# Kernel optimization log

Hardware: AMD Instinct MI355X
Metric: run time of the kernel (lower is better)

## Reference

```python
import jax, jax.numpy as jnp
import numpy as np
import math

EMBED_DIM = 1024
NUM_HEADS = 16
HEAD_DIM = EMBED_DIM // NUM_HEADS          # 64
SUB_HEAD_DIM = HEAD_DIM // 2               # 32
SCALING = 1.0 / math.sqrt(SUB_HEAD_DIM)
LAMBDA_INIT = 0.8 - 0.6 * math.exp(-0.3 * 0)  # layer_idx = 0 -> 0.2


def setup_inputs() -> dict:
    key = jax.random.key(0)
    ks = jax.random.split(key, 10)
    B, T, D = 2, 2048, EMBED_DIM
    xav = math.sqrt(6.0 / (D + D))  # xavier_uniform bound for square-ish mats
    return {
        "query": jax.random.normal(ks[0], (B, T, D), jnp.float32),
        "key": jax.random.normal(ks[1], (B, T, D), jnp.float32),
        "value": jax.random.normal(ks[2], (B, T, D), jnp.float32),
        "in_proj_weight": jax.random.uniform(ks[3], (3 * D, D), jnp.float32, -xav, xav),
        "in_proj_bias": jnp.zeros((3 * D,), jnp.float32),
        "out_proj_weight": jax.random.uniform(ks[4], (D, D), jnp.float32, -xav, xav),
        "out_proj_bias": jnp.zeros((D,), jnp.float32),
        "lambda_q1": 0.1 * jax.random.normal(ks[5], (SUB_HEAD_DIM,), jnp.float32),
        "lambda_k1": 0.1 * jax.random.normal(ks[6], (SUB_HEAD_DIM,), jnp.float32),
        "lambda_q2": 0.1 * jax.random.normal(ks[7], (SUB_HEAD_DIM,), jnp.float32),
        "lambda_k2": 0.1 * jax.random.normal(ks[8], (SUB_HEAD_DIM,), jnp.float32),
    }


def reference(query, key, value, in_proj_weight, in_proj_bias,
              out_proj_weight, out_proj_bias,
              lambda_q1, lambda_k1, lambda_q2, lambda_k2):
    B, T, D = query.shape
    S = key.shape[1]
    H, hd, sd = NUM_HEADS, HEAD_DIM, SUB_HEAD_DIM

    qw, kw, vw = jnp.split(in_proj_weight, 3, axis=0)
    qb, kb, vb = jnp.split(in_proj_bias, 3, axis=0)
    q = query @ qw.T + qb
    k = key @ kw.T + kb
    v = value @ vw.T + vb

    # [B, H, T, head_dim]
    q = q.reshape(B, T, H, hd).transpose(0, 2, 1, 3)
    k = k.reshape(B, S, H, hd).transpose(0, 2, 1, 3)
    v = v.reshape(B, S, H, hd).transpose(0, 2, 1, 3)

    q1, q2 = q[..., :sd], q[..., sd:]
    k1, k2 = k[..., :sd], k[..., sd:]

    logits_1 = jnp.einsum('bhtd,bhsd->bhts', q1, k1) * SCALING
    logits_2 = jnp.einsum('bhtd,bhsd->bhts', q2, k2) * SCALING

    a1 = jax.nn.softmax(logits_1, axis=-1)
    a2 = jax.nn.softmax(logits_2, axis=-1)

    lam = (jnp.exp(jnp.dot(lambda_q1, lambda_k1))
           - jnp.exp(jnp.dot(lambda_q2, lambda_k2)) + LAMBDA_INIT)

    diff_weights = a1 - lam * a2
    attn_output = jnp.einsum('bhts,bhsd->bhtd', diff_weights, v)
    attn_output = attn_output * (1.0 - LAMBDA_INIT)

    attn_output = attn_output.transpose(0, 2, 1, 3).reshape(B, T, D)
    output = attn_output @ out_proj_weight.T + out_proj_bias
    return output
```

## Files before the change

kernel.cpp:

```cpp
#include <hip/hip_runtime.h>
#include <cstdint>
#include <cstddef>

typedef unsigned short u16;
typedef __attribute__((ext_vector_type(8))) short bf16x8;
typedef __attribute__((ext_vector_type(4))) short bf16x4;
typedef __attribute__((ext_vector_type(4))) float f32x4;

__device__ __forceinline__ u16 f2bf(float f) {
  uint32_t u = __float_as_uint(f);
  u += 0x7fffu + ((u >> 16) & 1u);
  return (u16)(u >> 16);
}

__device__ __forceinline__ short f2bfs(float f) {
  __bf16 h = (__bf16)f;
  return __builtin_bit_cast(short, h);
}

__device__ __forceinline__ float bf2f(u16 u) {
  return __uint_as_float(((uint32_t)u) << 16);
}

#define MFMA16(a, b, c) __builtin_amdgcn_mfma_f32_16x16x32_bf16((a), (b), (c), 0, 0, 0)

__device__ __forceinline__ float ex2(float x) {
#if __has_builtin(__builtin_amdgcn_exp2f)
  return __builtin_amdgcn_exp2f(x);
#else
  return exp2f(x);
#endif
}

__global__ __launch_bounds__(256) void cvt3_kernel(const float* __restrict__ q,
                                                   const float* __restrict__ k,
                                                   const float* __restrict__ v,
                                                   u16* __restrict__ out, int n8) {
  int i = blockIdx.x * blockDim.x + threadIdx.x;
  if (i >= n8) return;
  const float* src = blockIdx.y == 0 ? q : (blockIdx.y == 1 ? k : v);
  u16* dst = out + (size_t)blockIdx.y * n8 * 8;
  const float4* p = (const float4*)src;
  float4 a = p[i * 2], b = p[i * 2 + 1];
  u16 o[8] = {f2bf(a.x), f2bf(a.y), f2bf(a.z), f2bf(a.w),
              f2bf(b.x), f2bf(b.y), f2bf(b.z), f2bf(b.w)};
  *(int4*)(dst + (size_t)i * 8) = *(const int4*)o;
}

__global__ __launch_bounds__(256) void cvtw_kernel(const float* __restrict__ w0,
                                                   const float* __restrict__ w1,
                                                   u16* __restrict__ o0,
                                                   u16* __restrict__ o1,
                                                   int n8_0, int n8_1) {
  int i = blockIdx.x * blockDim.x + threadIdx.x;
  const float* src;
  u16* dst;
  if (blockIdx.y == 0) {
    if (i >= n8_0) return;
    src = w0; dst = o0;
  } else {
    if (i >= n8_1) return;
    src = w1; dst = o1;
  }
  const float4* p = (const float4*)src;
  float4 a = p[i * 2], b = p[i * 2 + 1];
  u16 o[8] = {f2bf(a.x), f2bf(a.y), f2bf(a.z), f2bf(a.w),
              f2bf(b.x), f2bf(b.y), f2bf(b.z), f2bf(b.w)};
  *(int4*)(dst + (size_t)i * 8) = *(const int4*)o;
}

template <typename OUT_T, bool SPLIT_A>
__global__ __launch_bounds__(256) void gemm_bt(const u16* __restrict__ Abase,
                                               const u16* __restrict__ B,
                                               const float* __restrict__ bias,
                                               OUT_T* __restrict__ C,
                                               u16* __restrict__ QH, u16* __restrict__ KH,
                                               u16* __restrict__ VT,
                                               int M, int N, int K) {
  __shared__ u16 As[128][68];
  __shared__ u16 Bs[128][68];
  const int nb = blockIdx.x, mb = blockIdx.y;
  const int t = threadIdx.x;
  const u16* A = Abase + (SPLIT_A ? (size_t)(nb >> 3) * (size_t)M * K : (size_t)0);
  const int w = t >> 6, lane = t & 63;
  const int wr = w >> 1, wc = w & 1;
  const int lr = lane & 15, lk = lane >> 4;
  const f32x4 zero4 = {0.f, 0.f, 0.f, 0.f};
  f32x4 acc[4][4];
#pragma unroll
  for (int i = 0; i < 4; ++i)
#pragma unroll
    for (int j = 0; j < 4; ++j) acc[i][j] = zero4;

  const int srow = t >> 3;
  const int scol = (t & 7) << 3;
  const u16* Ap = A + (size_t)(mb * 128 + srow) * K + scol;
  const u16* Bp = B + (size_t)(nb * 128 + srow) * K + scol;

  for (int k0 = 0; k0 < K; k0 += 64) {
    __syncthreads();
#pragma unroll
    for (int j = 0; j < 4; ++j) {
      *(int4*)&As[srow + 32 * j][scol] = *(const int4*)(Ap + (size_t)(32 * j) * K + k0);
      *(int4*)&Bs[srow + 32 * j][scol] = *(const int4*)(Bp + (size_t)(32 * j) * K + k0);
    }
    __syncthreads();
#pragma unroll
    for (int kk = 0; kk < 2; ++kk) {
      bf16x8 af[4], bfr[4];
#pragma unroll
      for (int mf = 0; mf < 4; ++mf)
        af[mf] = *(const bf16x8*)&As[wr * 64 + mf * 16 + lr][kk * 32 + lk * 8];
#pragma unroll
      for (int nf = 0; nf < 4; ++nf)
        bfr[nf] = *(const bf16x8*)&Bs[wc * 64 + nf * 16 + lr][kk * 32 + lk * 8];
#pragma unroll
      for (int mf = 0; mf < 4; ++mf)
#pragma unroll
        for (int nf = 0; nf < 4; ++nf) acc[mf][nf] = MFMA16(af[mf], bfr[nf], acc[mf][nf]);
    }
  }

  if constexpr (SPLIT_A) {
    const int third = nb >> 3;
    const int bb = mb >> 4;
#pragma unroll
    for (int nf = 0; nf < 4; ++nf) {
      const int col = nb * 128 + wc * 64 + nf * 16 + lr;
      const int c = col & 1023;
      const int h = c >> 6, d = c & 63;
      const float bv = bias[col];
      u16* qk = (third == 0 ? QH : KH) + (size_t)(bb * 16 + h) * 2048 * 64;
      u16* vt = VT + ((size_t)(bb * 16 + h) * 64 + d) * 2048;
#pragma unroll
      for (int mf = 0; mf < 4; ++mf) {
        const int row0 = mb * 128 + wr * 64 + mf * 16 + lk * 4;
        const int s0 = row0 & 2047;
        if (third < 2) {
#pragma unroll
          for (int r = 0; r < 4; ++r)
            qk[(size_t)(s0 + r) * 64 + d] = f2bf(acc[mf][nf][r] + bv);
        } else {
          u16 tmp[4];
#pragma unroll
          for (int r = 0; r < 4; ++r) tmp[r] = f2bf(acc[mf][nf][r] + bv);
          *(uint2*)&vt[s0] = *(const uint2*)tmp;
        }
      }
    }
  } else {
#pragma unroll
    for (int nf = 0; nf < 4; ++nf) {
      const int col = nb * 128 + wc * 64 + nf * 16 + lr;
      const float bv = bias[col];
#pragma unroll
      for (int mf = 0; mf < 4; ++mf) {
        const int row0 = mb * 128 + wr * 64 + mf * 16 + lk * 4;
#pragma unroll
        for (int r = 0; r < 4; ++r)
          ((float*)C)[(size_t)(row0 + r) * N + col] = acc[mf][nf][r] + bv;
      }
    }
  }
}

__global__ __launch_bounds__(512, 2) void diff_attn(const u16* __restrict__ QH,
                                                    const u16* __restrict__ KH,
                                                    const u16* __restrict__ VT,
                                                    const float* __restrict__ lq1,
                                                    const float* __restrict__ lk1,
                                                    const float* __restrict__ lq2,
                                                    const float* __restrict__ lk2,
                                                    u16* __restrict__ ATTN) {
  __shared__ u16 Ks[64][68];
  __shared__ u16 Vs[64][68];
  const int t = threadIdx.x;
  const int id = blockIdx.x;
  const int swz = (id & 7) * 64 + (id >> 3);
  const int qt = swz & 15, bh = swz >> 4;
  const int b = bh >> 4, h = bh & 15;
  const int w = t >> 6, lane = t & 63;
  const int lr = lane & 15, lk = lane >> 4;
  const float QSC = 0.17677669529663687f * 1.4426950408889634f;

  float dd1 = 0.f, dd2 = 0.f;
  for (int i = 0; i < 32; ++i) { dd1 += lq1[i] * lk1[i]; dd2 += lq2[i] * lk2[i]; }
  const float lam = __expf(dd1) - __expf(dd2) + 0.2f;

  const int srow = t >> 3;
  const int scol = (t & 7) << 3;
  const int krow = (srow & 32) | ((srow & 4) << 2) | ((srow & 24) >> 1) | (srow & 3);
  const u16* qh = QH + (size_t)(b * 16 + h) * 2048 * 64;
  const u16* kh = KH + (size_t)(b * 16 + h) * 2048 * 64;
  const u16* vt = VT + (size_t)(b * 16 + h) * 64 * 2048;

  bf16x8 qa[2];
#pragma unroll
  for (int hh = 0; hh < 2; ++hh) {
    bf16x8 q = *(const bf16x8*)(qh + (size_t)(qt * 128 + w * 16 + lr) * 64 + hh * 32 + lk * 8);
#pragma unroll
    for (int i = 0; i < 8; ++i) q[i] = f2bfs(bf2f((u16)q[i]) * QSC);
    qa[hh] = q;
  }

  const f32x4 zero4 = {0.f, 0.f, 0.f, 0.f};
  f32x4 O[2][4], Ol[2];
#pragma unroll
  for (int hh = 0; hh < 2; ++hh) {
    Ol[hh] = zero4;
#pragma unroll
    for (int df = 0; df < 4; ++df) O[hh][df] = zero4;
  }
  bf16x8 vone8;
#pragma unroll
  for (int i = 0; i < 8; ++i) vone8[i] = (short)0x3F80;

  const u16* kp = kh + (size_t)srow * 64 + scol;
  const u16* vp = vt + (size_t)srow * 2048 + scol;

  int4 kA = *(const int4*)kp;
  int4 vA = *(const int4*)vp;
  int4 kB, vB;

  for (int it = 0; it < 32; ++it) {
    __syncthreads();
    *(int4*)&Ks[krow][scol] = kA;
    *(int4*)&Vs[srow][scol] = vA;
    if (it < 31) {
      const int s1 = (it + 1) * 64;
      kB = *(const int4*)(kp + (size_t)s1 * 64);
      vB = *(const int4*)(vp + s1);
    }
    __syncthreads();

    bf16x8 pk8[2][2];
#pragma unroll
    for (int hh = 0; hh < 2; ++hh) {
      f32x4 St[4];
#pragma unroll
      for (int nf = 0; nf < 4; ++nf) {
        bf16x8 kb = *(const bf16x8*)&Ks[nf * 16 + lr][hh * 32 + lk * 8];
        St[nf] = MFMA16(kb, qa[hh], zero4);
      }
#pragma unroll
      for (int j = 0; j < 2; ++j) {
        bf16x8 p;
#pragma unroll
        for (int a = 0; a < 2; ++a)
#pragma unroll
          for (int r = 0; r < 4; ++r)
            p[a * 4 + r] = f2bfs(ex2(St[2 * j + a][r]));
        pk8[hh][j] = p;
      }
    }

    __builtin_amdgcn_s_setprio(1);
#pragma unroll
    for (int j = 0; j < 2; ++j) {
      const bf16x8 pa0 = pk8[0][j], pa1 = pk8[1][j];
#pragma unroll
      for (int df = 0; df < 4; ++df) {
        bf16x8 vb = *(const bf16x8*)&Vs[df * 16 + lr][j * 32 + lk * 8];
        O[0][df] = MFMA16(pa0, vb, O[0][df]);
        O[1][df] = MFMA16(pa1, vb, O[1][df]);
      }
      Ol[0] = MFMA16(pa0, vone8, Ol[0]);
      Ol[1] = MFMA16(pa1, vone8, Ol[1]);
    }
    __builtin_amdgcn_s_setprio(0);

    kA = kB; vA = vB;
  }

  float i1[4], i2[4];
#pragma unroll
  for (int r = 0; r < 4; ++r) {
    i1[r] = 1.f / Ol[0][r];
    i2[r] = 1.f / Ol[1][r];
  }
  const size_t qrow0 = (size_t)b * 2048 + (size_t)qt * 128;
#pragma unroll
  for (int df = 0; df < 4; ++df) {
    const int col = h * 64 + df * 16 + lr;
#pragma unroll
    for (int r = 0; r < 4; ++r) {
      const size_t row = qrow0 + w * 16 + lk * 4 + r;
      float v = 0.8f * (O[0][df][r] * i1[r] - lam * O[1][df][r] * i2[r]);
      ATTN[row * 1024 + col] = f2bf(v);
    }
  }
}

extern "C" void kernel_launch(void* const* d_in, const int* in_sizes, int n_in,
                              void* d_out, int out_size, void* d_ws, size_t ws_size,
                              hipStream_t stream) {
  (void)in_sizes; (void)n_in; (void)out_size; (void)ws_size;
  const float* query = (const float*)d_in[0];
  const float* key_  = (const float*)d_in[1];
  const float* value = (const float*)d_in[2];
  const float* ipw   = (const float*)d_in[3];
  const float* ipb   = (const float*)d_in[4];
  const float* opw   = (const float*)d_in[5];
  const float* opb   = (const float*)d_in[6];
  const float* lq1   = (const float*)d_in[7];
  const float* lk1   = (const float*)d_in[8];
  const float* lq2   = (const float*)d_in[9];
  const float* lk2   = (const float*)d_in[10];

  const int M = 4096, D = 1024;
  u16* X    = (u16*)d_ws;
  u16* Wqkv = X + (size_t)3 * M * D;
  u16* Wout = Wqkv + (size_t)3 * D * D;
  u16* QH   = Wout + (size_t)D * D;
  u16* KH   = QH + (size_t)M * D;
  u16* VT   = KH + (size_t)M * D;
  u16* ATTN = VT + (size_t)M * D;

  {
    int n8 = (int)((size_t)M * D / 8);
    cvt3_kernel<<<dim3((n8 + 255) / 256, 3), dim3(256), 0, stream>>>(
        query, key_, value, X, n8);
  }
  {
    int n8_0 = (int)((size_t)3 * D * D / 8);
    int n8_1 = (int)((size_t)D * D / 8);
    cvtw_kernel<<<dim3((n8_0 + 255) / 256, 2), dim3(256), 0, stream>>>(
        ipw, opw, Wqkv, Wout, n8_0, n8_1);
  }

  gemm_bt<u16, true><<<dim3(24, 32), dim3(256), 0, stream>>>(
      X, Wqkv, ipb, (u16*)nullptr, QH, KH, VT, M, 3 * D, D);
  diff_attn<<<dim3(512), dim3(512), 0, stream>>>(QH, KH, VT, lq1, lk1, lq2, lk2, ATTN);
  gemm_bt<float, false><<<dim3(8, 32), dim3(256), 0, stream>>>(
      ATTN, Wout, opb, (float*)d_out, nullptr, nullptr, nullptr, M, D, D);
}
```

Before: 140.0 us.

## Merge conversion kernels, retile output GEMM to 128x64, prioritize QK MFMAs

The two fp32-to-bf16 conversion kernels become one five-way launch, removing a kernel launch. The output projection gets its own GEMM kernel with a 128x64 tile, doubling the block count from 256 to 512 so more of the GPU's compute units are busy. The attention loop also raises wave priority around the QK MFMA issue. In exchange, the smaller output tile has lower arithmetic intensity and reloads more A data per block.

```diff
diff --git a/kernel.cpp b/kernel.cpp
--- a/kernel.cpp
+++ b/kernel.cpp
@@ -32,14 +32,30 @@
 #endif
 }
 
-__global__ __launch_bounds__(256) void cvt3_kernel(const float* __restrict__ q,
+__global__ __launch_bounds__(256) void cvt5_kernel(const float* __restrict__ q,
                                                    const float* __restrict__ k,
                                                    const float* __restrict__ v,
-                                                   u16* __restrict__ out, int n8) {
+                                                   const float* __restrict__ w0,
+                                                   const float* __restrict__ w1,
+                                                   u16* __restrict__ X,
+                                                   u16* __restrict__ Wqkv,
+                                                   u16* __restrict__ Wout,
+                                                   int n8i, int n8w, int n8o) {
   int i = blockIdx.x * blockDim.x + threadIdx.x;
-  if (i >= n8) return;
-  const float* src = blockIdx.y == 0 ? q : (blockIdx.y == 1 ? k : v);
-  u16* dst = out + (size_t)blockIdx.y * n8 * 8;
+  const int y = blockIdx.y;
+  const float* src;
+  u16* dst;
+  if (y < 3) {
+    if (i >= n8i) return;
+    src = (y == 0) ? q : (y == 1 ? k : v);
+    dst = X + (size_t)y * n8i * 8;
+  } else if (y == 3) {
+    if (i >= n8w) return;
+    src = w0; dst = Wqkv;
+  } else {
+    if (i >= n8o) return;
+    src = w1; dst = Wout;
+  }
   const float4* p = (const float4*)src;
   float4 a = p[i * 2], b = p[i * 2 + 1];
   u16 o[8] = {f2bf(a.x), f2bf(a.y), f2bf(a.z), f2bf(a.w),
@@ -47,41 +63,17 @@
   *(int4*)(dst + (size_t)i * 8) = *(const int4*)o;
 }
 
-__global__ __launch_bounds__(256) void cvtw_kernel(const float* __restrict__ w0,
-                                                   const float* __restrict__ w1,
-                                                   u16* __restrict__ o0,
-                                                   u16* __restrict__ o1,
-                                                   int n8_0, int n8_1) {
-  int i = blockIdx.x * blockDim.x + threadIdx.x;
-  const float* src;
-  u16* dst;
-  if (blockIdx.y == 0) {
-    if (i >= n8_0) return;
-    src = w0; dst = o0;
-  } else {
-    if (i >= n8_1) return;
-    src = w1; dst = o1;
-  }
-  const float4* p = (const float4*)src;
-  float4 a = p[i * 2], b = p[i * 2 + 1];
-  u16 o[8] = {f2bf(a.x), f2bf(a.y), f2bf(a.z), f2bf(a.w),
-              f2bf(b.x), f2bf(b.y), f2bf(b.z), f2bf(b.w)};
-  *(int4*)(dst + (size_t)i * 8) = *(const int4*)o;
-}
-
-template <typename OUT_T, bool SPLIT_A>
-__global__ __launch_bounds__(256) void gemm_bt(const u16* __restrict__ Abase,
-                                               const u16* __restrict__ B,
-                                               const float* __restrict__ bias,
-                                               OUT_T* __restrict__ C,
-                                               u16* __restrict__ QH, u16* __restrict__ KH,
-                                               u16* __restrict__ VT,
-                                               int M, int N, int K) {
+__global__ __launch_bounds__(256) void gemm_qkv(const u16* __restrict__ Abase,
+                                                const u16* __restrict__ B,
+                                                const float* __restrict__ bias,
+                                                u16* __restrict__ QH, u16* __restrict__ KH,
+                                                u16* __restrict__ VT,
+                                                int M, int N, int K) {
   __shared__ u16 As[128][68];
   __shared__ u16 Bs[128][68];
   const int nb = blockIdx.x, mb = blockIdx.y;
   const int t = threadIdx.x;
-  const u16* A = Abase + (SPLIT_A ? (size_t)(nb >> 3) * (size_t)M * K : (size_t)0);
+  const u16* A = Abase + (size_t)(nb >> 3) * (size_t)M * K;
   const int w = t >> 6, lane = t & 63;
   const int wr = w >> 1, wc = w & 1;
   const int lr = lane & 15, lk = lane >> 4;
@@ -121,45 +113,92 @@
     }
   }
 
-  if constexpr (SPLIT_A) {
-    const int third = nb >> 3;
-    const int bb = mb >> 4;
-#pragma unroll
-    for (int nf = 0; nf < 4; ++nf) {
-      const int col = nb * 128 + wc * 64 + nf * 16 + lr;
-      const int c = col & 1023;
-      const int h = c >> 6, d = c & 63;
-      const float bv = bias[col];
-      u16* qk = (third == 0 ? QH : KH) + (size_t)(bb * 16 + h) * 2048 * 64;
-      u16* vt = VT + ((size_t)(bb * 16 + h) * 64 + d) * 2048;
-#pragma unroll
-      for (int mf = 0; mf < 4; ++mf) {
-        const int row0 = mb * 128 + wr * 64 + mf * 16 + lk * 4;
-        const int s0 = row0 & 2047;
-        if (third < 2) {
-#pragma unroll
-          for (int r = 0; r < 4; ++r)
-            qk[(size_t)(s0 + r) * 64 + d] = f2bf(acc[mf][nf][r] + bv);
-        } else {
-          u16 tmp[4];
-#pragma unroll
-          for (int r = 0; r < 4; ++r) tmp[r] = f2bf(acc[mf][nf][r] + bv);
-          *(uint2*)&vt[s0] = *(const uint2*)tmp;
-        }
+  const int third = nb >> 3;
+  const int bb = mb >> 4;
+#pragma unroll
+  for (int nf = 0; nf < 4; ++nf) {
+    const int col = nb * 128 + wc * 64 + nf * 16 + lr;
+    const int c = col & 1023;
+    const int h = c >> 6, d = c & 63;
+    const float bv = bias[col];
+    u16* qk = (third == 0 ? QH : KH) + (size_t)(bb * 16 + h) * 2048 * 64;
+    u16* vt = VT + ((size_t)(bb * 16 + h) * 64 + d) * 2048;
+#pragma unroll
+    for (int mf = 0; mf < 4; ++mf) {
+      const int row0 = mb * 128 + wr * 64 + mf * 16 + lk * 4;
+      const int s0 = row0 & 2047;
+      if (third < 2) {
+#pragma unroll
+        for (int r = 0; r < 4; ++r)
+          qk[(size_t)(s0 + r) * 64 + d] = f2bf(acc[mf][nf][r] + bv);
+      } else {
+        u16 tmp[4];
+#pragma unroll
+        for (int r = 0; r < 4; ++r) tmp[r] = f2bf(acc[mf][nf][r] + bv);
+        *(uint2*)&vt[s0] = *(const uint2*)tmp;
       }
     }
-  } else {
-#pragma unroll
-    for (int nf = 0; nf < 4; ++nf) {
-      const int col = nb * 128 + wc * 64 + nf * 16 + lr;
-      const float bv = bias[col];
-#pragma unroll
-      for (int mf = 0; mf < 4; ++mf) {
-        const int row0 = mb * 128 + wr * 64 + mf * 16 + lk * 4;
-#pragma unroll
-        for (int r = 0; r < 4; ++r)
-          ((float*)C)[(size_t)(row0 + r) * N + col] = acc[mf][nf][r] + bv;
-      }
+  }
+}
+
+__global__ __launch_bounds__(256) void gemm_out(const u16* __restrict__ A,
+                                                const u16* __restrict__ B,
+                                                const float* __restrict__ bias,
+                                                float* __restrict__ C,
+                                                int M, int N, int K) {
+  __shared__ u16 As[128][68];
+  __shared__ u16 Bs[64][68];
+  const int nb = blockIdx.x, mb = blockIdx.y;
+  const int t = threadIdx.x;
+  const int w = t >> 6, lane = t & 63;
+  const int lr = lane & 15, lk = lane >> 4;
+  const f32x4 zero4 = {0.f, 0.f, 0.f, 0.f};
+  f32x4 acc[2][4];
+#pragma unroll
+  for (int i = 0; i < 2; ++i)
+#pragma unroll
+    for (int j = 0; j < 4; ++j) acc[i][j] = zero4;
+
+  const int srow = t >> 3;
+  const int scol = (t & 7) << 3;
+  const u16* Ap = A + (size_t)(mb * 128 + srow) * K + scol;
+  const u16* Bp = B + (size_t)(nb * 64 + srow) * K + scol;
+
+  for (int k0 = 0; k0 < K; k0 += 64) {
+    __syncthreads();
+#pragma unroll
+    for (int j = 0; j < 4; ++j)
+      *(int4*)&As[srow + 32 * j][scol] = *(const int4*)(Ap + (size_t)(32 * j) * K + k0);
+#pragma unroll
+    for (int j = 0; j < 2; ++j)
+      *(int4*)&Bs[srow + 32 * j][scol] = *(const int4*)(Bp + (size_t)(32 * j) * K + k0);
+    __syncthreads();
+#pragma unroll
+    for (int kk = 0; kk < 2; ++kk) {
+      bf16x8 af[2], bfr[4];
+#pragma unroll
+      for (int mf = 0; mf < 2; ++mf)
+        af[mf] = *(const bf16x8*)&As[w * 32 + mf * 16 + lr][kk * 32 + lk * 8];
+#pragma unroll
+      for (int nf = 0; nf < 4; ++nf)
+        bfr[nf] = *(const bf16x8*)&Bs[nf * 16 + lr][kk * 32 + lk * 8];
+#pragma unroll
+      for (int mf = 0; mf < 2; ++mf)
+#pragma unroll
+        for (int nf = 0; nf < 4; ++nf) acc[mf][nf] = MFMA16(af[mf], bfr[nf], acc[mf][nf]);
+    }
+  }
+
+#pragma unroll
+  for (int nf = 0; nf < 4; ++nf) {
+    const int col = nb * 64 + nf * 16 + lr;
+    const float bv = bias[col];
+#pragma unroll
+    for (int mf = 0; mf < 2; ++mf) {
+      const int row0 = mb * 128 + w * 32 + mf * 16 + lk * 4;
+#pragma unroll
+      for (int r = 0; r < 4; ++r)
+        C[(size_t)(row0 + r) * N + col] = acc[mf][nf][r] + bv;
     }
   }
 }
@@ -237,11 +276,13 @@
 #pragma unroll
     for (int hh = 0; hh < 2; ++hh) {
       f32x4 St[4];
+      __builtin_amdgcn_s_setprio(1);
 #pragma unroll
       for (int nf = 0; nf < 4; ++nf) {
         bf16x8 kb = *(const bf16x8*)&Ks[nf * 16 + lr][hh * 32 + lk * 8];
         St[nf] = MFMA16(kb, qa[hh], zero4);
       }
+      __builtin_amdgcn_s_setprio(0);
 #pragma unroll
       for (int j = 0; j < 2; ++j) {
         bf16x8 p;
@@ -317,20 +358,16 @@
   u16* ATTN = VT + (size_t)M * D;
 
   {
-    int n8 = (int)((size_t)M * D / 8);
-    cvt3_kernel<<<dim3((n8 + 255) / 256, 3), dim3(256), 0, stream>>>(
-        query, key_, value, X, n8);
-  }
-  {
-    int n8_0 = (int)((size_t)3 * D * D / 8);
-    int n8_1 = (int)((size_t)D * D / 8);
-    cvtw_kernel<<<dim3((n8_0 + 255) / 256, 2), dim3(256), 0, stream>>>(
-        ipw, opw, Wqkv, Wout, n8_0, n8_1);
-  }
-
-  gemm_bt<u16, true><<<dim3(24, 32), dim3(256), 0, stream>>>(
-      X, Wqkv, ipb, (u16*)nullptr, QH, KH, VT, M, 3 * D, D);
+    int n8i = (int)((size_t)M * D / 8);
+    int n8w = (int)((size_t)3 * D * D / 8);
+    int n8o = (int)((size_t)D * D / 8);
+    cvt5_kernel<<<dim3((n8i + 255) / 256, 5), dim3(256), 0, stream>>>(
+        query, key_, value, ipw, opw, X, Wqkv, Wout, n8i, n8w, n8o);
+  }
+
+  gemm_qkv<<<dim3(24, 32), dim3(256), 0, stream>>>(
+      X, Wqkv, ipb, QH, KH, VT, M, 3 * D, D);
   diff_attn<<<dim3(512), dim3(512), 0, stream>>>(QH, KH, VT, lq1, lk1, lq2, lk2, ATTN);
-  gemm_bt<float, false><<<dim3(8, 32), dim3(256), 0, stream>>>(
-      ATTN, Wout, opb, (float*)d_out, nullptr, nullptr, nullptr, M, D, D);
-}
+  gemm_out<<<dim3(16, 32), dim3(256), 0, stream>>>(
+      ATTN, Wout, opb, (float*)d_out, M, D, D);
+}
```

New measurement: 135.2 us (median of 3 runs). 1.03x faster.
